# Kernel tuning notes

Measured on AMD Instinct MI355X. Metric: run time of the kernel, lower is better.

## Reference

```python
import jax, jax.numpy as jnp
import numpy as np

B, H, S, D = 2, 16, 2048, 128


def setup_inputs() -> dict:
    key = jax.random.key(0)
    kq, kk, kv = jax.random.split(key, 3)
    q = jax.random.normal(kq, (B, H, S, D), dtype=jnp.float32)
    k = jax.random.normal(kk, (B, H, S, D), dtype=jnp.float32)
    v = jax.random.normal(kv, (B, H, S, D), dtype=jnp.float32)
    return {"q": q, "k": k, "v": v}


def reference(q, k, v):
    # cp_size == 1 path: causal scaled dot-product attention.
    # Identical math to the ring online-softmax accumulation collapsed to one step.
    d = q.shape[-1]
    scale = d ** -0.5
    scores = jnp.einsum("bhsd,bhtd->bhst", q, k) * scale  # (B,H,S,S)
    s = scores.shape[-1]
    causal_mask = jnp.tril(jnp.ones((s, s), dtype=bool))  # (S,S)
    scores = jnp.where(causal_mask, scores, -jnp.inf)
    probs = jax.nn.softmax(scores, axis=-1)
    return jnp.einsum("bhst,bhtd->bhsd", probs, v)
```

## Files before the change

kernel.cpp:

```cpp
#include <hip/hip_runtime.h>
#include <hip/hip_bf16.h>

constexpr int Bb = 2, Hh = 16, Ss = 2048, Dd = 128;
constexpr int BM = 128, BN = 64;
constexpr int NQT = Ss / BM;
constexpr float SCALE = 0.088388347648318447f * 1.4426950408889634f;

typedef __attribute__((ext_vector_type(8))) short bf16x8;
typedef __attribute__((ext_vector_type(16))) float f32x16;
typedef __attribute__((ext_vector_type(4))) int int4v;

__device__ __forceinline__ unsigned cvtpk(float lo, float hi) {
  unsigned r;
  asm("v_cvt_pk_bf16_f32 %0, %1, %2" : "=v"(r) : "v"(lo), "v"(hi));
  return r;
}
__device__ __forceinline__ float exp2hw(float x) {
  float r;
  asm("v_exp_f32 %0, %1" : "=v"(r) : "v"(x));
  return r;
}
__device__ __forceinline__ void permswap(unsigned &x, unsigned &y) {
  asm("v_permlane32_swap_b32 %0, %1" : "+v"(x), "+v"(y));
}
__device__ __forceinline__ float fcomp(float4 f, int j) {
  return j == 0 ? f.x : (j == 1 ? f.y : (j == 2 ? f.z : f.w));
}
__device__ __forceinline__ void block_sync_lds() {
  __builtin_amdgcn_sched_barrier(0);
  asm volatile("s_waitcnt lgkmcnt(0)" ::: "memory");
  __builtin_amdgcn_s_barrier();
  __builtin_amdgcn_sched_barrier(0);
}

__global__ __launch_bounds__(256, 2)
void fa_fwd_kernel(const float* __restrict__ q, const float* __restrict__ k,
                   const float* __restrict__ v, float* __restrict__ out) {
  __shared__ __align__(16) char Klds[2][BN * 256];
  __shared__ __align__(16) char Vlds[2][Dd * 128];

  const int tid = threadIdx.x;
  const int wave = tid >> 6, lane = tid & 63;
  const int l31 = lane & 31, hi = lane >> 5, hi4 = hi * 4;
  const int bid = blockIdx.x;
  const int bh = bid & 31;
  const int r2 = bid >> 5;
  const int qt = (r2 < 8) ? (15 - r2) : (r2 - 8);

  const float* qb = q + (size_t)bh * Ss * Dd;
  const float* kb = k + (size_t)bh * Ss * Dd;
  const float* vb = v + (size_t)bh * Ss * Dd;

  const int qv = wave * 32 + l31;

  bf16x8 qf[8];
  {
    const float* qr = qb + (size_t)(qt * BM + qv) * Dd + hi * 8;
    #pragma unroll
    for (int ks = 0; ks < 8; ++ks) {
      float4 a = *(const float4*)(qr + ks * 16);
      float4 b = *(const float4*)(qr + ks * 16 + 4);
      int4v t;
      t[0] = (int)cvtpk(a.x * SCALE, a.y * SCALE);
      t[1] = (int)cvtpk(a.z * SCALE, a.w * SCALE);
      t[2] = (int)cvtpk(b.x * SCALE, b.y * SCALE);
      t[3] = (int)cvtpk(b.z * SCALE, b.w * SCALE);
      qf[ks] = __builtin_bit_cast(bf16x8, t);
    }
  }

  const int krow0 = tid >> 4;
  const int kblk  = tid & 15;
  const int kswz  = kblk ^ krow0;
  const int vkg = tid >> 5;
  const int vdq = tid & 31;

  float4 ka[4], kc[4];
  float4 vr[8];

  auto load_k = [&](int kt) {
    const float* Kg = kb + (size_t)(kt * BN) * Dd + kblk * 8;
    #pragma unroll
    for (int i = 0; i < 4; ++i) {
      ka[i] = *(const float4*)(Kg + (size_t)(krow0 + 16 * i) * Dd);
      kc[i] = *(const float4*)(Kg + (size_t)(krow0 + 16 * i) * Dd + 4);
    }
  };
  auto load_v = [&](int kt) {
    const float* Vg = vb + (size_t)(kt * BN + vkg * 8) * Dd + vdq * 4;
    #pragma unroll
    for (int r = 0; r < 8; ++r)
      vr[r] = *(const float4*)(Vg + (size_t)r * Dd);
  };

  auto stage_k = [&](char* Kb) {
    #pragma unroll
    for (int i = 0; i < 4; ++i) {
      int4v t;
      t[0] = (int)cvtpk(ka[i].x, ka[i].y);
      t[1] = (int)cvtpk(ka[i].z, ka[i].w);
      t[2] = (int)cvtpk(kc[i].x, kc[i].y);
      t[3] = (int)cvtpk(kc[i].z, kc[i].w);
      *(int4v*)(Kb + (krow0 + 16 * i) * 256 + kswz * 16) = t;
    }
  };
  auto stage_v = [&](char* Vb) {
    #pragma unroll
    for (int j = 0; j < 4; ++j) {
      int d = vdq * 4 + j;
      int f7 = (d ^ (d >> 3)) & 7;
      int4v t;
      t[0] = (int)cvtpk(fcomp(vr[0], j), fcomp(vr[1], j));
      t[1] = (int)cvtpk(fcomp(vr[2], j), fcomp(vr[3], j));
      t[2] = (int)cvtpk(fcomp(vr[4], j), fcomp(vr[5], j));
      t[3] = (int)cvtpk(fcomp(vr[6], j), fcomp(vr[7], j));
      *(int4v*)(Vb + d * 128 + (vkg ^ f7) * 16) = t;
    }
  };

  f32x16 o[4];
  #pragma unroll
  for (int i = 0; i < 4; ++i) o[i] = (f32x16)(0.0f);
  float mrow = -3.0e38f, lrow = 0.0f;

  const int nkt = 2 * qt + 2;

  load_k(0); load_v(0);
  stage_k(&Klds[0][0]); stage_v(&Vlds[0][0]);
  load_k(1); load_v(1);

  for (int kt = 0; kt < nkt; ++kt) {
    block_sync_lds();
    const int cur = kt & 1;
    const char* Kc = &Klds[cur][0];
    const char* Vc = &Vlds[cur][0];
    const bool more = kt + 1 < nkt;
    const int kn = (kt + 2 < nkt) ? kt + 2 : nkt - 1;

    const int thr = qt * 128 + qv - kt * 64;
    const bool live = (qt * 128 + wave * 32 + 31 - kt * 64) >= 0;

    bf16x8 pf[4];
    if (live) {
      f32x16 acc[2];
      acc[0] = (f32x16)(0.0f); acc[1] = (f32x16)(0.0f);
      __builtin_amdgcn_s_setprio(1);
      #pragma unroll
      for (int ks = 0; ks < 8; ++ks) {
        #pragma unroll
        for (int t = 0; t < 2; ++t) {
          int row = t * 32 + l31;
          int bswz = (2 * ks + hi) ^ (row & 15);
          bf16x8 kf = *(const bf16x8*)(Kc + row * 256 + bswz * 16);
          acc[t] = __builtin_amdgcn_mfma_f32_32x32x16_bf16(kf, qf[ks], acc[t], 0, 0, 0);
        }
      }
      __builtin_amdgcn_s_setprio(0);

      if (kt + 2 >= nkt) {
        #pragma unroll
        for (int t = 0; t < 2; ++t)
          #pragma unroll
          for (int r = 0; r < 16; ++r) {
            int key = t * 32 + (r & 3) + 8 * (r >> 2) + hi4;
            if (key > thr) acc[t][r] = -1.0e30f;
          }
      }

      float mp0 = acc[0][0], mp1 = acc[0][1], mp2 = acc[0][2], mp3 = acc[0][3];
      #pragma unroll
      for (int t = 0; t < 2; ++t)
        #pragma unroll
        for (int r = (t == 0 ? 4 : 0); r < 16; r += 4) {
          mp0 = fmaxf(mp0, acc[t][r + 0]);
          mp1 = fmaxf(mp1, acc[t][r + 1]);
          mp2 = fmaxf(mp2, acc[t][r + 2]);
          mp3 = fmaxf(mp3, acc[t][r + 3]);
        }
      float mx = fmaxf(fmaxf(mp0, mp1), fmaxf(mp2, mp3));
      mx = fmaxf(mx, __shfl_xor(mx, 32, 64));

      if (!__all(mx - mrow <= 8.0f)) {
        float mn = fmaxf(mrow, mx);
        float al = exp2hw(mrow - mn);
        mrow = mn;
        lrow *= al;
        #pragma unroll
        for (int dt = 0; dt < 4; ++dt)
          #pragma unroll
          for (int r = 0; r < 16; ++r) o[dt][r] *= al;
      }

      float rp0 = 0.f, rp1 = 0.f, rp2 = 0.f, rp3 = 0.f;
      #pragma unroll
      for (int t = 0; t < 2; ++t)
        #pragma unroll
        for (int r = 0; r < 16; r += 4) {
          float p0 = exp2hw(acc[t][r + 0] - mrow);
          float p1 = exp2hw(acc[t][r + 1] - mrow);
          float p2 = exp2hw(acc[t][r + 2] - mrow);
          float p3 = exp2hw(acc[t][r + 3] - mrow);
          acc[t][r + 0] = p0; acc[t][r + 1] = p1;
          acc[t][r + 2] = p2; acc[t][r + 3] = p3;
          rp0 += p0; rp1 += p1; rp2 += p2; rp3 += p3;
        }
      lrow += (rp0 + rp1) + (rp2 + rp3);

      #pragma unroll
      for (int ks2 = 0; ks2 < 4; ++ks2) {
        int t = ks2 >> 1, s8 = (ks2 & 1) * 8;
        unsigned A0 = cvtpk(acc[t][s8 + 0], acc[t][s8 + 1]);
        unsigned A1 = cvtpk(acc[t][s8 + 2], acc[t][s8 + 3]);
        unsigned B0 = cvtpk(acc[t][s8 + 4], acc[t][s8 + 5]);
        unsigned B1 = cvtpk(acc[t][s8 + 6], acc[t][s8 + 7]);
        permswap(A0, B0);
        permswap(A1, B1);
        int4v pw; pw[0] = (int)A0; pw[1] = (int)A1; pw[2] = (int)B0; pw[3] = (int)B1;
        pf[ks2] = __builtin_bit_cast(bf16x8, pw);
      }
    }

    if (more) {
      __builtin_amdgcn_sched_barrier(0);
      stage_k(&Klds[cur ^ 1][0]);
      load_k(kn);
      __builtin_amdgcn_sched_barrier(0);
    }

    if (live) {
      __builtin_amdgcn_s_setprio(1);
      #pragma unroll
      for (int dt = 0; dt < 4; ++dt) {
        int row = dt * 32 + l31;
        int f7 = (row ^ (row >> 3)) & 7;
        #pragma unroll
        for (int ks2 = 0; ks2 < 4; ++ks2) {
          int bswz = (2 * ks2 + hi) ^ f7;
          bf16x8 vf = *(const bf16x8*)(Vc + row * 128 + bswz * 16);
          o[dt] = __builtin_amdgcn_mfma_f32_32x32x16_bf16(vf, pf[ks2], o[dt], 0, 0, 0);
        }
      }
      __builtin_amdgcn_s_setprio(0);
    }

    if (more) {
      __builtin_amdgcn_sched_barrier(0);
      stage_v(&Vlds[cur ^ 1][0]);
      load_v(kn);
    }
  }

  lrow += __shfl_xor(lrow, 32, 64);
  const float linv = 1.0f / lrow;
  float* ob = out + ((size_t)bh * Ss + qt * BM + qv) * Dd;
  #pragma unroll
  for (int dt = 0; dt < 4; ++dt)
    #pragma unroll
    for (int g = 0; g < 4; ++g) {
      float4 w;
      w.x = o[dt][g * 4 + 0] * linv;
      w.y = o[dt][g * 4 + 1] * linv;
      w.z = o[dt][g * 4 + 2] * linv;
      w.w = o[dt][g * 4 + 3] * linv;
      *(float4*)(ob + dt * 32 + g * 8 + hi4) = w;
    }
}

extern "C" void kernel_launch(void* const* d_in, const int* in_sizes, int n_in,
                              void* d_out, int out_size, void* d_ws, size_t ws_size,
                              hipStream_t stream) {
  const float* q = (const float*)d_in[0];
  const float* k = (const float*)d_in[1];
  const float* v = (const float*)d_in[2];
  float* out = (float*)d_out;
  dim3 grid(Bb * Hh * NQT);
  dim3 block(256);
  hipLaunchKernelGGL(fa_fwd_kernel, grid, block, 0, stream, q, k, v, out);
}
```

Measured before the change: 183.9 us.

## Split causal attention rows into balanced KV segments with a merge kernel

Each batch-head's causal workload is split into 16 roughly equal chunks, following static segment tables over (q-tile, kv-range). This balances per-block work instead of leaving blocks with anywhere from 2 to 32 KV tiles. Segments that cover only part of a q-tile's KV range write unnormalized partial outputs plus row max and row sum to a workspace. A second kernel then merges those partials with softmax rescaling. The KV prefetch is also simplified from two tiles ahead to one, and the split path depends on a large workspace being available, falling back to the old grid otherwise.

```diff
diff --git a/kernel.cpp b/kernel.cpp
--- a/kernel.cpp
+++ b/kernel.cpp
@@ -9,6 +9,13 @@
 typedef __attribute__((ext_vector_type(8))) short bf16x8;
 typedef __attribute__((ext_vector_type(16))) float f32x16;
 typedef __attribute__((ext_vector_type(4))) int int4v;
+
+__device__ const int SEG_OFF[17] = {0,4,7,9,11,13,15,17,19,20,22,24,25,27,28,30,31};
+__device__ const int SEG_QT[31]  = {0,1,2,3, 3,4,5, 5,6, 6,7, 7,8, 8,9, 9,10, 10,11, 11, 11,12, 12,13, 13, 13,14, 14, 14,15, 15};
+__device__ const int SEG_K0[31]  = {0,0,0,0, 5,0,0, 4,0, 9,0, 12,0, 13,0, 12,0, 9,0, 4, 21,0, 14,0, 5, 22,0, 11, 28,0, 15};
+__device__ const int SEG_K1[31]  = {2,4,6,5, 8,10,4, 12,9, 14,12, 16,13, 18,12, 20,9, 22,4, 21, 24,14, 26,5, 22, 28,11, 28, 30,15, 32};
+__device__ const int SEG_LOC[31] = {0,0,0,0, 1,0,0, 1,0, 1,0, 1,0, 1,0, 1,0, 1,0, 1, 2,0, 1,0, 1, 2,0, 1, 2,0, 1};
+__device__ const int QT_NSEG[16] = {1,1,1,2,1,2,2,2,2,2,2,3,2,3,3,2};
 
 __device__ __forceinline__ unsigned cvtpk(float lo, float hi) {
   unsigned r;
@@ -34,8 +41,9 @@
 }
 
 __global__ __launch_bounds__(256, 2)
-void fa_fwd_kernel(const float* __restrict__ q, const float* __restrict__ k,
-                   const float* __restrict__ v, float* __restrict__ out) {
+void fa_seg_kernel(const float* __restrict__ q, const float* __restrict__ k,
+                   const float* __restrict__ v, float* __restrict__ out,
+                   float* __restrict__ wsO, float* __restrict__ wsML) {
   __shared__ __align__(16) char Klds[2][BN * 256];
   __shared__ __align__(16) char Vlds[2][Dd * 128];
 
@@ -43,37 +51,27 @@
   const int wave = tid >> 6, lane = tid & 63;
   const int l31 = lane & 31, hi = lane >> 5, hi4 = hi * 4;
   const int bid = blockIdx.x;
-  const int bh = bid & 31;
-  const int r2 = bid >> 5;
-  const int qt = (r2 < 8) ? (15 - r2) : (r2 - 8);
+  const bool wsmode = (wsO != nullptr);
+
+  int bh, si0, si1, qt_fb = 0;
+  if (wsmode) {
+    bh = bid >> 4;
+    const int chunk = bid & 15;
+    si0 = SEG_OFF[chunk]; si1 = SEG_OFF[chunk + 1];
+  } else {
+    bh = bid & 31;
+    const int r2 = bid >> 5;
+    qt_fb = (r2 < 8) ? (15 - r2) : (r2 - 8);
+    si0 = 0; si1 = 1;
+  }
 
   const float* qb = q + (size_t)bh * Ss * Dd;
   const float* kb = k + (size_t)bh * Ss * Dd;
   const float* vb = v + (size_t)bh * Ss * Dd;
-
-  const int qv = wave * 32 + l31;
-
-  bf16x8 qf[8];
-  {
-    const float* qr = qb + (size_t)(qt * BM + qv) * Dd + hi * 8;
-    #pragma unroll
-    for (int ks = 0; ks < 8; ++ks) {
-      float4 a = *(const float4*)(qr + ks * 16);
-      float4 b = *(const float4*)(qr + ks * 16 + 4);
-      int4v t;
-      t[0] = (int)cvtpk(a.x * SCALE, a.y * SCALE);
-      t[1] = (int)cvtpk(a.z * SCALE, a.w * SCALE);
-      t[2] = (int)cvtpk(b.x * SCALE, b.y * SCALE);
-      t[3] = (int)cvtpk(b.z * SCALE, b.w * SCALE);
-      qf[ks] = __builtin_bit_cast(bf16x8, t);
-    }
-  }
-
-  const int krow0 = tid >> 4;
-  const int kblk  = tid & 15;
-  const int kswz  = kblk ^ krow0;
-  const int vkg = tid >> 5;
-  const int vdq = tid & 31;
+  const int qloc = wave * 32 + l31;
+
+  const int krow0 = tid >> 4, kblk = tid & 15, kswz = kblk ^ krow0;
+  const int vkg = tid >> 5, vdq = tid & 31;
 
   float4 ka[4], kc[4];
   float4 vr[8];
@@ -92,7 +90,6 @@
     for (int r = 0; r < 8; ++r)
       vr[r] = *(const float4*)(Vg + (size_t)r * Dd);
   };
-
   auto stage_k = [&](char* Kb) {
     #pragma unroll
     for (int i = 0; i < 4; ++i) {
@@ -118,152 +115,230 @@
     }
   };
 
-  f32x16 o[4];
-  #pragma unroll
-  for (int i = 0; i < 4; ++i) o[i] = (f32x16)(0.0f);
-  float mrow = -3.0e38f, lrow = 0.0f;
-
-  const int nkt = 2 * qt + 2;
-
-  load_k(0); load_v(0);
-  stage_k(&Klds[0][0]); stage_v(&Vlds[0][0]);
-  load_k(1); load_v(1);
-
-  for (int kt = 0; kt < nkt; ++kt) {
-    block_sync_lds();
-    const int cur = kt & 1;
-    const char* Kc = &Klds[cur][0];
-    const char* Vc = &Vlds[cur][0];
-    const bool more = kt + 1 < nkt;
-    const int kn = (kt + 2 < nkt) ? kt + 2 : nkt - 1;
-
-    const int thr = qt * 128 + qv - kt * 64;
-    const bool live = (qt * 128 + wave * 32 + 31 - kt * 64) >= 0;
-
-    bf16x8 pf[4];
-    if (live) {
-      f32x16 acc[2];
-      acc[0] = (f32x16)(0.0f); acc[1] = (f32x16)(0.0f);
-      __builtin_amdgcn_s_setprio(1);
+  for (int si = si0; si < si1; ++si) {
+    const int qt  = wsmode ? SEG_QT[si] : qt_fb;
+    const int kt0 = wsmode ? SEG_K0[si] : 0;
+    const int nkt = 2 * qt + 2;
+    const int kte = wsmode ? SEG_K1[si] : nkt;
+    const int loc = wsmode ? SEG_LOC[si] : 0;
+    const bool isfull = (kt0 == 0) && (kte == nkt);
+    const int nloc = kte - kt0;
+
+    bf16x8 qf[8];
+    {
+      const float* qr = qb + (size_t)(qt * BM + qloc) * Dd + hi * 8;
       #pragma unroll
       for (int ks = 0; ks < 8; ++ks) {
-        #pragma unroll
-        for (int t = 0; t < 2; ++t) {
-          int row = t * 32 + l31;
-          int bswz = (2 * ks + hi) ^ (row & 15);
-          bf16x8 kf = *(const bf16x8*)(Kc + row * 256 + bswz * 16);
-          acc[t] = __builtin_amdgcn_mfma_f32_32x32x16_bf16(kf, qf[ks], acc[t], 0, 0, 0);
-        }
+        float4 a = *(const float4*)(qr + ks * 16);
+        float4 b = *(const float4*)(qr + ks * 16 + 4);
+        int4v t;
+        t[0] = (int)cvtpk(a.x * SCALE, a.y * SCALE);
+        t[1] = (int)cvtpk(a.z * SCALE, a.w * SCALE);
+        t[2] = (int)cvtpk(b.x * SCALE, b.y * SCALE);
+        t[3] = (int)cvtpk(b.z * SCALE, b.w * SCALE);
+        qf[ks] = __builtin_bit_cast(bf16x8, t);
       }
-      __builtin_amdgcn_s_setprio(0);
-
-      if (kt + 2 >= nkt) {
+    }
+
+    f32x16 o[4];
+    #pragma unroll
+    for (int i = 0; i < 4; ++i) o[i] = (f32x16)(0.0f);
+    float mrow = -3.0e38f, lrow = 0.0f;
+
+    load_k(kt0); load_v(kt0);
+    block_sync_lds();
+    stage_k(&Klds[0][0]); stage_v(&Vlds[0][0]);
+
+    for (int i = 0; i < nloc; ++i) {
+      block_sync_lds();
+      const int kt = kt0 + i;
+      const int cur = i & 1;
+      const char* Kc = &Klds[cur][0];
+      const char* Vc = &Vlds[cur][0];
+      const bool more = i + 1 < nloc;
+      if (more) load_k(kt + 1);
+
+      const int thr = qt * 128 + qloc - kt * 64;
+      const bool live = (qt * 128 + wave * 32 + 31 - kt * 64) >= 0;
+
+      bf16x8 pf[4];
+      if (live) {
+        f32x16 acc[2];
+        acc[0] = (f32x16)(0.0f); acc[1] = (f32x16)(0.0f);
+        __builtin_amdgcn_s_setprio(1);
+        #pragma unroll
+        for (int ks = 0; ks < 8; ++ks) {
+          #pragma unroll
+          for (int t = 0; t < 2; ++t) {
+            int row = t * 32 + l31;
+            int bswz = (2 * ks + hi) ^ (row & 15);
+            bf16x8 kf = *(const bf16x8*)(Kc + row * 256 + bswz * 16);
+            acc[t] = __builtin_amdgcn_mfma_f32_32x32x16_bf16(kf, qf[ks], acc[t], 0, 0, 0);
+          }
+        }
+        __builtin_amdgcn_s_setprio(0);
+
+        if (kt + 2 >= nkt) {
+          #pragma unroll
+          for (int t = 0; t < 2; ++t)
+            #pragma unroll
+            for (int r = 0; r < 16; ++r) {
+              int key = t * 32 + (r & 3) + 8 * (r >> 2) + hi4;
+              if (key > thr) acc[t][r] = -1.0e30f;
+            }
+        }
+
+        float mp0 = acc[0][0], mp1 = acc[0][1], mp2 = acc[0][2], mp3 = acc[0][3];
         #pragma unroll
         for (int t = 0; t < 2; ++t)
           #pragma unroll
-          for (int r = 0; r < 16; ++r) {
-            int key = t * 32 + (r & 3) + 8 * (r >> 2) + hi4;
-            if (key > thr) acc[t][r] = -1.0e30f;
+          for (int r = (t == 0 ? 4 : 0); r < 16; r += 4) {
+            mp0 = fmaxf(mp0, acc[t][r + 0]);
+            mp1 = fmaxf(mp1, acc[t][r + 1]);
+            mp2 = fmaxf(mp2, acc[t][r + 2]);
+            mp3 = fmaxf(mp3, acc[t][r + 3]);
           }
+        float mx = fmaxf(fmaxf(mp0, mp1), fmaxf(mp2, mp3));
+        mx = fmaxf(mx, __shfl_xor(mx, 32, 64));
+
+        if (!__all(mx - mrow <= 8.0f)) {
+          float mn = fmaxf(mrow, mx);
+          float al = exp2hw(mrow - mn);
+          mrow = mn;
+          lrow *= al;
+          #pragma unroll
+          for (int dt = 0; dt < 4; ++dt)
+            #pragma unroll
+            for (int r = 0; r < 16; ++r) o[dt][r] *= al;
+        }
+
+        float rp0 = 0.f, rp1 = 0.f, rp2 = 0.f, rp3 = 0.f;
+        #pragma unroll
+        for (int t = 0; t < 2; ++t)
+          #pragma unroll
+          for (int r = 0; r < 16; r += 4) {
+            float p0 = exp2hw(acc[t][r + 0] - mrow);
+            float p1 = exp2hw(acc[t][r + 1] - mrow);
+            float p2 = exp2hw(acc[t][r + 2] - mrow);
+            float p3 = exp2hw(acc[t][r + 3] - mrow);
+            acc[t][r + 0] = p0; acc[t][r + 1] = p1;
+            acc[t][r + 2] = p2; acc[t][r + 3] = p3;
+            rp0 += p0; rp1 += p1; rp2 += p2; rp3 += p3;
+          }
+        lrow += (rp0 + rp1) + (rp2 + rp3);
+
+        #pragma unroll
+        for (int ks2 = 0; ks2 < 4; ++ks2) {
+          int t = ks2 >> 1, s8 = (ks2 & 1) * 8;
+          unsigned A0 = cvtpk(acc[t][s8 + 0], acc[t][s8 + 1]);
+          unsigned A1 = cvtpk(acc[t][s8 + 2], acc[t][s8 + 3]);
+          unsigned B0 = cvtpk(acc[t][s8 + 4], acc[t][s8 + 5]);
+          unsigned B1 = cvtpk(acc[t][s8 + 6], acc[t][s8 + 7]);
+          permswap(A0, B0);
+          permswap(A1, B1);
+          int4v pw; pw[0] = (int)A0; pw[1] = (int)A1; pw[2] = (int)B0; pw[3] = (int)B1;
+          pf[ks2] = __builtin_bit_cast(bf16x8, pw);
+        }
       }
 
-      float mp0 = acc[0][0], mp1 = acc[0][1], mp2 = acc[0][2], mp3 = acc[0][3];
+      if (more) stage_k(&Klds[cur ^ 1][0]);
+      __builtin_amdgcn_sched_barrier(0);
+      if (more) load_v(kt + 1);
+
+      if (live) {
+        __builtin_amdgcn_s_setprio(1);
+        #pragma unroll
+        for (int dt = 0; dt < 4; ++dt) {
+          int row = dt * 32 + l31;
+          int f7 = (row ^ (row >> 3)) & 7;
+          #pragma unroll
+          for (int ks2 = 0; ks2 < 4; ++ks2) {
+            int bswz = (2 * ks2 + hi) ^ f7;
+            bf16x8 vf = *(const bf16x8*)(Vc + row * 128 + bswz * 16);
+            o[dt] = __builtin_amdgcn_mfma_f32_32x32x16_bf16(vf, pf[ks2], o[dt], 0, 0, 0);
+          }
+        }
+        __builtin_amdgcn_s_setprio(0);
+      }
+
+      if (more) stage_v(&Vlds[cur ^ 1][0]);
+    }
+
+    float lsum = lrow + __shfl_xor(lrow, 32, 64);
+    if (isfull) {
+      const float linv = 1.0f / lsum;
+      float* ob = out + ((size_t)bh * Ss + qt * BM + qloc) * Dd;
       #pragma unroll
-      for (int t = 0; t < 2; ++t)
-        #pragma unroll
-        for (int r = (t == 0 ? 4 : 0); r < 16; r += 4) {
-          mp0 = fmaxf(mp0, acc[t][r + 0]);
-          mp1 = fmaxf(mp1, acc[t][r + 1]);
-          mp2 = fmaxf(mp2, acc[t][r + 2]);
-          mp3 = fmaxf(mp3, acc[t][r + 3]);
-        }
-      float mx = fmaxf(fmaxf(mp0, mp1), fmaxf(mp2, mp3));
-      mx = fmaxf(mx, __shfl_xor(mx, 32, 64));
-
-      if (!__all(mx - mrow <= 8.0f)) {
-        float mn = fmaxf(mrow, mx);
-        float al = exp2hw(mrow - mn);
-        mrow = mn;
-        lrow *= al;
-        #pragma unroll
-        for (int dt = 0; dt < 4; ++dt)
-          #pragma unroll
-          for (int r = 0; r < 16; ++r) o[dt][r] *= al;
+      for (int dt = 0; dt < 4; ++dt)
+        #pragma unroll
+        for (int g = 0; g < 4; ++g) {
+          float4 w;
+          w.x = o[dt][g * 4 + 0] * linv;
+          w.y = o[dt][g * 4 + 1] * linv;
+          w.z = o[dt][g * 4 + 2] * linv;
+          w.w = o[dt][g * 4 + 3] * linv;
+          *(float4*)(ob + dt * 32 + g * 8 + hi4) = w;
+        }
+    } else {
+      const int slot = (bh * 16 + qt) * 3 + loc;
+      float* po = wsO + (size_t)slot * 16384 + (size_t)qloc * 128;
+      #pragma unroll
+      for (int dt = 0; dt < 4; ++dt)
+        #pragma unroll
+        for (int g = 0; g < 4; ++g) {
+          float4 w;
+          w.x = o[dt][g * 4 + 0]; w.y = o[dt][g * 4 + 1];
+          w.z = o[dt][g * 4 + 2]; w.w = o[dt][g * 4 + 3];
+          *(float4*)(po + dt * 32 + g * 8 + hi4) = w;
+        }
+      if (hi == 0) {
+        wsML[(size_t)slot * 256 + qloc]       = mrow;
+        wsML[(size_t)slot * 256 + 128 + qloc] = lsum;
       }
-
-      float rp0 = 0.f, rp1 = 0.f, rp2 = 0.f, rp3 = 0.f;
-      #pragma unroll
-      for (int t = 0; t < 2; ++t)
-        #pragma unroll
-        for (int r = 0; r < 16; r += 4) {
-          float p0 = exp2hw(acc[t][r + 0] - mrow);
-          float p1 = exp2hw(acc[t][r + 1] - mrow);
-          float p2 = exp2hw(acc[t][r + 2] - mrow);
-          float p3 = exp2hw(acc[t][r + 3] - mrow);
-          acc[t][r + 0] = p0; acc[t][r + 1] = p1;
-          acc[t][r + 2] = p2; acc[t][r + 3] = p3;
-          rp0 += p0; rp1 += p1; rp2 += p2; rp3 += p3;
-        }
-      lrow += (rp0 + rp1) + (rp2 + rp3);
-
-      #pragma unroll
-      for (int ks2 = 0; ks2 < 4; ++ks2) {
-        int t = ks2 >> 1, s8 = (ks2 & 1) * 8;
-        unsigned A0 = cvtpk(acc[t][s8 + 0], acc[t][s8 + 1]);
-        unsigned A1 = cvtpk(acc[t][s8 + 2], acc[t][s8 + 3]);
-        unsigned B0 = cvtpk(acc[t][s8 + 4], acc[t][s8 + 5]);
-        unsigned B1 = cvtpk(acc[t][s8 + 6], acc[t][s8 + 7]);
-        permswap(A0, B0);
-        permswap(A1, B1);
-        int4v pw; pw[0] = (int)A0; pw[1] = (int)A1; pw[2] = (int)B0; pw[3] = (int)B1;
-        pf[ks2] = __builtin_bit_cast(bf16x8, pw);
-      }
-    }
-
-    if (more) {
-      __builtin_amdgcn_sched_barrier(0);
-      stage_k(&Klds[cur ^ 1][0]);
-      load_k(kn);
-      __builtin_amdgcn_sched_barrier(0);
-    }
-
-    if (live) {
-      __builtin_amdgcn_s_setprio(1);
-      #pragma unroll
-      for (int dt = 0; dt < 4; ++dt) {
-        int row = dt * 32 + l31;
-        int f7 = (row ^ (row >> 3)) & 7;
-        #pragma unroll
-        for (int ks2 = 0; ks2 < 4; ++ks2) {
-          int bswz = (2 * ks2 + hi) ^ f7;
-          bf16x8 vf = *(const bf16x8*)(Vc + row * 128 + bswz * 16);
-          o[dt] = __builtin_amdgcn_mfma_f32_32x32x16_bf16(vf, pf[ks2], o[dt], 0, 0, 0);
-        }
-      }
-      __builtin_amdgcn_s_setprio(0);
-    }
-
-    if (more) {
-      __builtin_amdgcn_sched_barrier(0);
-      stage_v(&Vlds[cur ^ 1][0]);
-      load_v(kn);
     }
   }
-
-  lrow += __shfl_xor(lrow, 32, 64);
-  const float linv = 1.0f / lrow;
-  float* ob = out + ((size_t)bh * Ss + qt * BM + qv) * Dd;
+}
+
+__global__ __launch_bounds__(256)
+void fa_merge_kernel(const float* __restrict__ wsO, const float* __restrict__ wsML,
+                     float* __restrict__ out) {
+  const int bid = blockIdx.x;
+  const int qt = bid & 15, bh = bid >> 4;
+  const int ns = QT_NSEG[qt];
+  if (ns < 2) return;
+  const int t = threadIdx.x;
+  const size_t s0 = (size_t)bid * 3;
+  const float* O0 = wsO + (s0 + 0) * 16384;
+  const float* O1 = wsO + (s0 + 1) * 16384;
+  const float* O2 = wsO + (s0 + 2) * 16384;
+  const float* M0 = wsML + (s0 + 0) * 256;
+  const float* M1 = wsML + (s0 + 1) * 256;
+  const float* M2 = wsML + (s0 + 2) * 256;
+  float* ob = out + ((size_t)bh * Ss + qt * 128) * Dd;
   #pragma unroll
-  for (int dt = 0; dt < 4; ++dt)
-    #pragma unroll
-    for (int g = 0; g < 4; ++g) {
-      float4 w;
-      w.x = o[dt][g * 4 + 0] * linv;
-      w.y = o[dt][g * 4 + 1] * linv;
-      w.z = o[dt][g * 4 + 2] * linv;
-      w.w = o[dt][g * 4 + 3] * linv;
-      *(float4*)(ob + dt * 32 + g * 8 + hi4) = w;
-    }
+  for (int i = 0; i < 16; ++i) {
+    int e4 = t + 256 * i;
+    int row = e4 >> 5, dof = (e4 & 31) * 4;
+    float m0 = M0[row], l0 = M0[128 + row];
+    float m1 = M1[row], l1 = M1[128 + row];
+    float m2 = -3.0e38f, l2 = 0.0f;
+    if (ns == 3) { m2 = M2[row]; l2 = M2[128 + row]; }
+    float M = fmaxf(fmaxf(m0, m1), m2);
+    float w0 = exp2hw(m0 - M), w1 = exp2hw(m1 - M);
+    float w2 = (ns == 3) ? exp2hw(m2 - M) : 0.0f;
+    float Li = 1.0f / (l0 * w0 + l1 * w1 + l2 * w2);
+    float4 a = *(const float4*)(O0 + (size_t)row * 128 + dof);
+    float4 b = *(const float4*)(O1 + (size_t)row * 128 + dof);
+    float4 r;
+    r.x = a.x * w0 + b.x * w1; r.y = a.y * w0 + b.y * w1;
+    r.z = a.z * w0 + b.z * w1; r.w = a.w * w0 + b.w * w1;
+    if (ns == 3) {
+      float4 c = *(const float4*)(O2 + (size_t)row * 128 + dof);
+      r.x += c.x * w2; r.y += c.y * w2; r.z += c.z * w2; r.w += c.w * w2;
+    }
+    r.x *= Li; r.y *= Li; r.z *= Li; r.w *= Li;
+    *(float4*)(ob + (size_t)row * Dd + dof) = r;
+  }
 }
 
 extern "C" void kernel_launch(void* const* d_in, const int* in_sizes, int n_in,
@@ -273,7 +348,14 @@
   const float* k = (const float*)d_in[1];
   const float* v = (const float*)d_in[2];
   float* out = (float*)d_out;
-  dim3 grid(Bb * Hh * NQT);
+  constexpr size_t SLOTS = 32 * 16 * 3;
+  constexpr size_t NEED_O  = SLOTS * 16384 * sizeof(float);
+  constexpr size_t NEED_ML = SLOTS * 256 * sizeof(float);
+  const bool split = (d_ws != nullptr) && (ws_size >= NEED_O + NEED_ML);
+  float* wsO  = split ? (float*)d_ws : nullptr;
+  float* wsML = split ? ((float*)d_ws + SLOTS * 16384) : nullptr;
   dim3 block(256);
-  hipLaunchKernelGGL(fa_fwd_kernel, grid, block, 0, stream, q, k, v, out);
-}
+  hipLaunchKernelGGL(fa_seg_kernel, dim3(512), block, 0, stream, q, k, v, out, wsO, wsML);
+  if (split)
+    hipLaunchKernelGGL(fa_merge_kernel, dim3(512), block, 0, stream, wsO, wsML, out);
+}
```

New measurement: 243.8 us. 32.6% more time.

## Split each key tile across two wave groups and merge partial softmax states

Applied to the files above, without the earlier changes.

Doubles the block to 512 threads so each pair of waves shares a 32-query slab and splits the 64-key tile in half, each wave computing its own scores and running max/sum over 32 keys. At the end the two partial softmax states are combined through an LDS exchange of max/sum and a swizzled output buffer before one wave writes the result. This is meant to raise wave-level parallelism and cut per-wave register pressure so occupancy can rise. In exchange it adds an end-of-kernel merge with extra barriers, doubles the Q fragment loads per block, and halves the per-thread global load width for K and V.

```diff
diff --git a/kernel.cpp b/kernel.cpp
--- a/kernel.cpp
+++ b/kernel.cpp
@@ -8,7 +8,9 @@
 
 typedef __attribute__((ext_vector_type(8))) short bf16x8;
 typedef __attribute__((ext_vector_type(16))) float f32x16;
+typedef __attribute__((ext_vector_type(4))) float f32x4v;
 typedef __attribute__((ext_vector_type(4))) int int4v;
+typedef __attribute__((ext_vector_type(2))) int int2v;
 
 __device__ __forceinline__ unsigned cvtpk(float lo, float hi) {
   unsigned r;
@@ -33,15 +35,16 @@
   __builtin_amdgcn_sched_barrier(0);
 }
 
-__global__ __launch_bounds__(256, 2)
+__global__ __launch_bounds__(512, 4)
 void fa_fwd_kernel(const float* __restrict__ q, const float* __restrict__ k,
                    const float* __restrict__ v, float* __restrict__ out) {
-  __shared__ __align__(16) char Klds[2][BN * 256];
-  __shared__ __align__(16) char Vlds[2][Dd * 128];
+  __shared__ __align__(16) char lds[65536];
+  __shared__ float2 mlbuf[8][64];
 
   const int tid = threadIdx.x;
   const int wave = tid >> 6, lane = tid & 63;
   const int l31 = lane & 31, hi = lane >> 5, hi4 = hi * 4;
+  const int qsub = wave >> 1, kg = wave & 1;
   const int bid = blockIdx.x;
   const int bh = bid & 31;
   const int r2 = bid >> 5;
@@ -50,8 +53,12 @@
   const float* qb = q + (size_t)bh * Ss * Dd;
   const float* kb = k + (size_t)bh * Ss * Dd;
   const float* vb = v + (size_t)bh * Ss * Dd;
-
-  const int qv = wave * 32 + l31;
+  const int qv = qsub * 32 + l31;
+
+  char* const Klds0 = lds;
+  char* const Klds1 = lds + 16384;
+  char* const Vlds0 = lds + 32768;
+  char* const Vlds1 = lds + 49152;
 
   bf16x8 qf[8];
   {
@@ -71,37 +78,36 @@
 
   const int krow0 = tid >> 4;
   const int kblk  = tid & 15;
-  const int kswz  = kblk ^ krow0;
+  const int kswz  = kblk ^ (krow0 & 15);
   const int vkg = tid >> 5;
   const int vdq = tid & 31;
 
-  float4 ka[4], kc[4];
-  float4 vr[8];
+  float4 ka[2], kc[2];
+  float4 vr[4];
 
   auto load_k = [&](int kt) {
     const float* Kg = kb + (size_t)(kt * BN) * Dd + kblk * 8;
     #pragma unroll
-    for (int i = 0; i < 4; ++i) {
-      ka[i] = *(const float4*)(Kg + (size_t)(krow0 + 16 * i) * Dd);
-      kc[i] = *(const float4*)(Kg + (size_t)(krow0 + 16 * i) * Dd + 4);
+    for (int i = 0; i < 2; ++i) {
+      ka[i] = *(const float4*)(Kg + (size_t)(krow0 + 32 * i) * Dd);
+      kc[i] = *(const float4*)(Kg + (size_t)(krow0 + 32 * i) * Dd + 4);
     }
   };
   auto load_v = [&](int kt) {
-    const float* Vg = vb + (size_t)(kt * BN + vkg * 8) * Dd + vdq * 4;
-    #pragma unroll
-    for (int r = 0; r < 8; ++r)
+    const float* Vg = vb + (size_t)(kt * BN + vkg * 4) * Dd + vdq * 4;
+    #pragma unroll
+    for (int r = 0; r < 4; ++r)
       vr[r] = *(const float4*)(Vg + (size_t)r * Dd);
   };
-
   auto stage_k = [&](char* Kb) {
     #pragma unroll
-    for (int i = 0; i < 4; ++i) {
+    for (int i = 0; i < 2; ++i) {
       int4v t;
       t[0] = (int)cvtpk(ka[i].x, ka[i].y);
       t[1] = (int)cvtpk(ka[i].z, ka[i].w);
       t[2] = (int)cvtpk(kc[i].x, kc[i].y);
       t[3] = (int)cvtpk(kc[i].z, kc[i].w);
-      *(int4v*)(Kb + (krow0 + 16 * i) * 256 + kswz * 16) = t;
+      *(int4v*)(Kb + (krow0 + 32 * i) * 256 + kswz * 16) = t;
     }
   };
   auto stage_v = [&](char* Vb) {
@@ -109,12 +115,10 @@
     for (int j = 0; j < 4; ++j) {
       int d = vdq * 4 + j;
       int f7 = (d ^ (d >> 3)) & 7;
-      int4v t;
+      int2v t;
       t[0] = (int)cvtpk(fcomp(vr[0], j), fcomp(vr[1], j));
       t[1] = (int)cvtpk(fcomp(vr[2], j), fcomp(vr[3], j));
-      t[2] = (int)cvtpk(fcomp(vr[4], j), fcomp(vr[5], j));
-      t[3] = (int)cvtpk(fcomp(vr[6], j), fcomp(vr[7], j));
-      *(int4v*)(Vb + d * 128 + (vkg ^ f7) * 16) = t;
+      *(int2v*)(Vb + d * 128 + ((vkg >> 1) ^ f7) * 16 + (vkg & 1) * 8) = t;
     }
   };
 
@@ -126,57 +130,50 @@
   const int nkt = 2 * qt + 2;
 
   load_k(0); load_v(0);
-  stage_k(&Klds[0][0]); stage_v(&Vlds[0][0]);
+  stage_k(Klds0); stage_v(Vlds0);
   load_k(1); load_v(1);
 
   for (int kt = 0; kt < nkt; ++kt) {
     block_sync_lds();
     const int cur = kt & 1;
-    const char* Kc = &Klds[cur][0];
-    const char* Vc = &Vlds[cur][0];
+    const char* Kc = cur ? Klds1 : Klds0;
+    const char* Vc = cur ? Vlds1 : Vlds0;
     const bool more = kt + 1 < nkt;
     const int kn = (kt + 2 < nkt) ? kt + 2 : nkt - 1;
 
-    const int thr = qt * 128 + qv - kt * 64;
-    const bool live = (qt * 128 + wave * 32 + 31 - kt * 64) >= 0;
-
-    bf16x8 pf[4];
+    const bool live = (qt * 128 + qsub * 32 + 31 - kt * 64 - kg * 32) >= 0;
+
+    bf16x8 pf[2];
     if (live) {
-      f32x16 acc[2];
-      acc[0] = (f32x16)(0.0f); acc[1] = (f32x16)(0.0f);
+      f32x16 acc = (f32x16)(0.0f);
+      const int krow = kg * 32 + l31;
+      const int kr15 = krow & 15;
       __builtin_amdgcn_s_setprio(1);
       #pragma unroll
       for (int ks = 0; ks < 8; ++ks) {
+        int bswz = (2 * ks + hi) ^ kr15;
+        bf16x8 kf = *(const bf16x8*)(Kc + krow * 256 + bswz * 16);
+        acc = __builtin_amdgcn_mfma_f32_32x32x16_bf16(kf, qf[ks], acc, 0, 0, 0);
+      }
+      __builtin_amdgcn_s_setprio(0);
+
+      if (kt + 2 >= nkt) {
+        const int thr2 = qt * 128 + qv - kt * 64 - kg * 32;
         #pragma unroll
-        for (int t = 0; t < 2; ++t) {
-          int row = t * 32 + l31;
-          int bswz = (2 * ks + hi) ^ (row & 15);
-          bf16x8 kf = *(const bf16x8*)(Kc + row * 256 + bswz * 16);
-          acc[t] = __builtin_amdgcn_mfma_f32_32x32x16_bf16(kf, qf[ks], acc[t], 0, 0, 0);
+        for (int r = 0; r < 16; ++r) {
+          int keyloc = (r & 3) + 8 * (r >> 2) + hi4;
+          if (keyloc > thr2) acc[r] = -1.0e30f;
         }
       }
-      __builtin_amdgcn_s_setprio(0);
-
-      if (kt + 2 >= nkt) {
-        #pragma unroll
-        for (int t = 0; t < 2; ++t)
-          #pragma unroll
-          for (int r = 0; r < 16; ++r) {
-            int key = t * 32 + (r & 3) + 8 * (r >> 2) + hi4;
-            if (key > thr) acc[t][r] = -1.0e30f;
-          }
-      }
-
-      float mp0 = acc[0][0], mp1 = acc[0][1], mp2 = acc[0][2], mp3 = acc[0][3];
-      #pragma unroll
-      for (int t = 0; t < 2; ++t)
-        #pragma unroll
-        for (int r = (t == 0 ? 4 : 0); r < 16; r += 4) {
-          mp0 = fmaxf(mp0, acc[t][r + 0]);
-          mp1 = fmaxf(mp1, acc[t][r + 1]);
-          mp2 = fmaxf(mp2, acc[t][r + 2]);
-          mp3 = fmaxf(mp3, acc[t][r + 3]);
-        }
+
+      float mp0 = acc[0], mp1 = acc[1], mp2 = acc[2], mp3 = acc[3];
+      #pragma unroll
+      for (int r = 4; r < 16; r += 4) {
+        mp0 = fmaxf(mp0, acc[r + 0]);
+        mp1 = fmaxf(mp1, acc[r + 1]);
+        mp2 = fmaxf(mp2, acc[r + 2]);
+        mp3 = fmaxf(mp3, acc[r + 3]);
+      }
       float mx = fmaxf(fmaxf(mp0, mp1), fmaxf(mp2, mp3));
       mx = fmaxf(mx, __shfl_xor(mx, 32, 64));
 
@@ -193,26 +190,24 @@
 
       float rp0 = 0.f, rp1 = 0.f, rp2 = 0.f, rp3 = 0.f;
       #pragma unroll
-      for (int t = 0; t < 2; ++t)
-        #pragma unroll
-        for (int r = 0; r < 16; r += 4) {
-          float p0 = exp2hw(acc[t][r + 0] - mrow);
-          float p1 = exp2hw(acc[t][r + 1] - mrow);
-          float p2 = exp2hw(acc[t][r + 2] - mrow);
-          float p3 = exp2hw(acc[t][r + 3] - mrow);
-          acc[t][r + 0] = p0; acc[t][r + 1] = p1;
-          acc[t][r + 2] = p2; acc[t][r + 3] = p3;
-          rp0 += p0; rp1 += p1; rp2 += p2; rp3 += p3;
-        }
+      for (int r = 0; r < 16; r += 4) {
+        float p0 = exp2hw(acc[r + 0] - mrow);
+        float p1 = exp2hw(acc[r + 1] - mrow);
+        float p2 = exp2hw(acc[r + 2] - mrow);
+        float p3 = exp2hw(acc[r + 3] - mrow);
+        acc[r + 0] = p0; acc[r + 1] = p1;
+        acc[r + 2] = p2; acc[r + 3] = p3;
+        rp0 += p0; rp1 += p1; rp2 += p2; rp3 += p3;
+      }
       lrow += (rp0 + rp1) + (rp2 + rp3);
 
       #pragma unroll
-      for (int ks2 = 0; ks2 < 4; ++ks2) {
-        int t = ks2 >> 1, s8 = (ks2 & 1) * 8;
-        unsigned A0 = cvtpk(acc[t][s8 + 0], acc[t][s8 + 1]);
-        unsigned A1 = cvtpk(acc[t][s8 + 2], acc[t][s8 + 3]);
-        unsigned B0 = cvtpk(acc[t][s8 + 4], acc[t][s8 + 5]);
-        unsigned B1 = cvtpk(acc[t][s8 + 6], acc[t][s8 + 7]);
+      for (int ks2 = 0; ks2 < 2; ++ks2) {
+        int s8 = ks2 * 8;
+        unsigned A0 = cvtpk(acc[s8 + 0], acc[s8 + 1]);
+        unsigned A1 = cvtpk(acc[s8 + 2], acc[s8 + 3]);
+        unsigned B0 = cvtpk(acc[s8 + 4], acc[s8 + 5]);
+        unsigned B1 = cvtpk(acc[s8 + 6], acc[s8 + 7]);
         permswap(A0, B0);
         permswap(A1, B1);
         int4v pw; pw[0] = (int)A0; pw[1] = (int)A1; pw[2] = (int)B0; pw[3] = (int)B1;
@@ -222,7 +217,7 @@
 
     if (more) {
       __builtin_amdgcn_sched_barrier(0);
-      stage_k(&Klds[cur ^ 1][0]);
+      stage_k(cur ? Klds0 : Klds1);
       load_k(kn);
       __builtin_amdgcn_sched_barrier(0);
     }
@@ -231,12 +226,12 @@
       __builtin_amdgcn_s_setprio(1);
       #pragma unroll
       for (int dt = 0; dt < 4; ++dt) {
-        int row = dt * 32 + l31;
-        int f7 = (row ^ (row >> 3)) & 7;
+        int rowd = dt * 32 + l31;
+        int f7 = (rowd ^ (rowd >> 3)) & 7;
         #pragma unroll
-        for (int ks2 = 0; ks2 < 4; ++ks2) {
-          int bswz = (2 * ks2 + hi) ^ f7;
-          bf16x8 vf = *(const bf16x8*)(Vc + row * 128 + bswz * 16);
+        for (int ks2 = 0; ks2 < 2; ++ks2) {
+          int bswz = (kg * 4 + 2 * ks2 + hi) ^ f7;
+          bf16x8 vf = *(const bf16x8*)(Vc + rowd * 128 + bswz * 16);
           o[dt] = __builtin_amdgcn_mfma_f32_32x32x16_bf16(vf, pf[ks2], o[dt], 0, 0, 0);
         }
       }
@@ -245,25 +240,52 @@
 
     if (more) {
       __builtin_amdgcn_sched_barrier(0);
-      stage_v(&Vlds[cur ^ 1][0]);
+      stage_v(cur ? Vlds0 : Vlds1);
       load_v(kn);
     }
   }
 
-  lrow += __shfl_xor(lrow, 32, 64);
-  const float linv = 1.0f / lrow;
-  float* ob = out + ((size_t)bh * Ss + qt * BM + qv) * Dd;
-  #pragma unroll
-  for (int dt = 0; dt < 4; ++dt)
-    #pragma unroll
-    for (int g = 0; g < 4; ++g) {
-      float4 w;
-      w.x = o[dt][g * 4 + 0] * linv;
-      w.y = o[dt][g * 4 + 1] * linv;
-      w.z = o[dt][g * 4 + 2] * linv;
-      w.w = o[dt][g * 4 + 3] * linv;
-      *(float4*)(ob + dt * 32 + g * 8 + hi4) = w;
-    }
+  float lsum = lrow + __shfl_xor(lrow, 32, 64);
+  mlbuf[wave][lane] = make_float2(mrow, lsum);
+  __syncthreads();
+  float2 ml1 = mlbuf[wave ^ 1][lane];
+  float M = fmaxf(mrow, ml1.x);
+  float w0 = exp2hw(mrow - M), w1 = exp2hw(ml1.x - M);
+  float ltot = lsum * w0 + ml1.y * w1;
+
+  char* const slab = lds + qsub * 16384;
+  if (kg == 1) {
+    #pragma unroll
+    for (int dt = 0; dt < 4; ++dt)
+      #pragma unroll
+      for (int g = 0; g < 4; ++g) {
+        int r16 = dt * 4 + g;
+        int blk = r16 ^ (l31 & 15);
+        f32x4v w;
+        w[0] = o[dt][g * 4 + 0]; w[1] = o[dt][g * 4 + 1];
+        w[2] = o[dt][g * 4 + 2]; w[3] = o[dt][g * 4 + 3];
+        *(f32x4v*)(slab + lane * 256 + blk * 16) = w;
+      }
+  }
+  __syncthreads();
+  if (kg == 0) {
+    const float linv = 1.0f / ltot;
+    float* ob = out + ((size_t)bh * Ss + qt * BM + qv) * Dd;
+    #pragma unroll
+    for (int dt = 0; dt < 4; ++dt)
+      #pragma unroll
+      for (int g = 0; g < 4; ++g) {
+        int r16 = dt * 4 + g;
+        int blk = r16 ^ (l31 & 15);
+        f32x4v o1 = *(const f32x4v*)(slab + lane * 256 + blk * 16);
+        float4 wv;
+        wv.x = (o[dt][g * 4 + 0] * w0 + o1[0] * w1) * linv;
+        wv.y = (o[dt][g * 4 + 1] * w0 + o1[1] * w1) * linv;
+        wv.z = (o[dt][g * 4 + 2] * w0 + o1[2] * w1) * linv;
+        wv.w = (o[dt][g * 4 + 3] * w0 + o1[3] * w1) * linv;
+        *(float4*)(ob + dt * 32 + g * 8 + hi4) = wv;
+      }
+  }
 }
 
 extern "C" void kernel_launch(void* const* d_in, const int* in_sizes, int n_in,
@@ -274,6 +296,6 @@
   const float* v = (const float*)d_in[2];
   float* out = (float*)d_out;
   dim3 grid(Bb * Hh * NQT);
-  dim3 block(256);
+  dim3 block(512);
   hipLaunchKernelGGL(fa_fwd_kernel, grid, block, 0, stream, q, k, v, out);
 }
```

Measured after the change: 412.4 us. 2.24x slower.
